# Performance work log

Hardware: AMD Instinct MI355X
Metric: run time of the kernel (lower is better)

The kernel has to match this reference:

```python
import jax, jax.numpy as jnp
import numpy as np

EPS_SHIFT = 1e-8   # additive epsilon used by the original code
EPS_NORM = 1e-12   # torch.nn.functional.normalize default eps


def setup_inputs() -> dict:
    key = jax.random.key(0)
    inputs = jax.random.normal(key, (1024, 2048, 3, 3), dtype=jnp.float32)
    return {"inputs": inputs}


def reference(inputs):
    # inputs: (B, num_res, 3, 3) -> flat atom chain (B, N, 3), N = 3*num_res
    B, R = inputs.shape[0], inputs.shape[1]
    x = inputs.reshape(B, R * 3, 3)

    # sliding 4-atom windows, vectorized over all N-3 dihedrals
    a = x[:, :-3, :]
    b = x[:, 1:-2, :]
    c = x[:, 2:-1, :]
    d = x[:, 3:, :]

    bc_raw = b - c + EPS_SHIFT
    bc = bc_raw / jnp.clip(
        jnp.linalg.norm(bc_raw, axis=-1, keepdims=True), EPS_NORM)

    n1 = jnp.cross(a - b, bc)          # (B, N-3, 3)
    n2 = jnp.cross(bc, c - d)          # (B, N-3, 3)
    xc = jnp.sum(n1 * n2, axis=-1)     # (B, N-3)
    yc = jnp.sum(jnp.cross(n1, bc) * n2, axis=-1)
    dih = jnp.arctan2(yc, xc + EPS_SHIFT)

    # original concatenates all sin values then all cos values along last dim
    angles = jnp.concatenate([jnp.sin(dih), jnp.cos(dih)], axis=-1)  # (B, 2*(N-3))
    first_three = x[:, :3, :]                                        # (B, 3, 3)
    return (angles, first_three)
```

## Files before the change

### kernel.cpp

```cpp
#include <hip/hip_runtime.h>

#define ROWS 1024
#define PTS 6144
#define NDIH (PTS - 3)
#define ROWF (PTS * 3)
#define CHUNK 256
#define NCHUNK ((NDIH + CHUNK - 1) / CHUNK)
#define ANG_PER_ROW (2 * NDIH)
#define EPS_SHIFT 1e-8f
#define EPS_NORM 1e-12f

__global__ __launch_bounds__(256) void dih_kernel(const float* __restrict__ in,
                                                  float* __restrict__ out) {
    __shared__ float s[(CHUNK + 3) * 3];
    const int b     = blockIdx.x / NCHUNK;
    const int chunk = blockIdx.x % NCHUNK;
    const int i0    = chunk * CHUNK;
    const int t     = threadIdx.x;

    const float* row = in + (size_t)b * ROWF;
    const int base = i0 * 3;
    const int cnt  = min((CHUNK + 3) * 3, ROWF - base);
    for (int k = t; k < cnt; k += CHUNK) s[k] = row[base + k];
    __syncthreads();

    if (chunk == 0 && t < 9) {
        out[(size_t)ROWS * ANG_PER_ROW + (size_t)b * 9 + t] = s[t];
    }

    const int i = i0 + t;
    if (i < NDIH) {
        const float* p = s + 3 * t;
        const float ax = p[0], ay = p[1],  az = p[2];
        const float bx = p[3], by = p[4],  bz = p[5];
        const float cx = p[6], cy = p[7],  cz = p[8];
        const float dx = p[9], dy = p[10], dz = p[11];

        const float brx = bx - cx + EPS_SHIFT;
        const float bry = by - cy + EPS_SHIFT;
        const float brz = bz - cz + EPS_SHIFT;
        const float nrm = sqrtf(brx*brx + bry*bry + brz*brz);
        const float inv = 1.0f / fmaxf(nrm, EPS_NORM);
        const float ux = brx * inv, uy = bry * inv, uz = brz * inv;

        const float abx = ax - bx, aby = ay - by, abz = az - bz;
        const float n1x = aby*uz - abz*uy;
        const float n1y = abz*ux - abx*uz;
        const float n1z = abx*uy - aby*ux;

        const float cdx = cx - dx, cdy = cy - dy, cdz = cz - dz;
        const float n2x = uy*cdz - uz*cdy;
        const float n2y = uz*cdx - ux*cdz;
        const float n2z = ux*cdy - uy*cdx;

        const float xc = n1x*n2x + n1y*n2y + n1z*n2z;

        const float mx = n1y*uz - n1z*uy;
        const float my = n1z*ux - n1x*uz;
        const float mz = n1x*uy - n1y*ux;
        const float yc = mx*n2x + my*n2y + mz*n2z;

        const float xz = xc + EPS_SHIFT;
        const float r2 = yc*yc + xz*xz;
        float s_, c_;
        if (r2 > 0.0f) {
            const float rinv = rsqrtf(r2);
            s_ = yc * rinv;
            c_ = xz * rinv;
        } else {
            s_ = 0.0f;
            c_ = 1.0f;
        }
        const size_t obase = (size_t)b * ANG_PER_ROW;
        out[obase + i]        = s_;
        out[obase + NDIH + i] = c_;
    }
}

extern "C" void kernel_launch(void* const* d_in, const int* in_sizes, int n_in,
                              void* d_out, int out_size, void* d_ws, size_t ws_size,
                              hipStream_t stream) {
    const float* in = (const float*)d_in[0];
    float* out = (float*)d_out;
    dih_kernel<<<dim3(ROWS * NCHUNK), dim3(CHUNK), 0, stream>>>(in, out);
}
```

Baseline: 139.5 us.

## Compute four dihedrals per thread with shared edge vectors and vectorized memory access

Each thread now computes four consecutive dihedrals from a 21-float register window. Bond differences are computed once and shared across adjacent dihedrals, and the chunk grows to 1024 dihedrals per 256-thread block. Global-to-shared staging and shared-to-register reads use float4, and sine outputs are written as float2 pairs. The aim is fewer instructions and memory transactions per dihedral, at the cost of higher register use per thread, fewer blocks, and a tail path for the last partial chunk.

```diff
diff --git a/kernel.cpp b/kernel.cpp
--- a/kernel.cpp
+++ b/kernel.cpp
@@ -4,15 +4,17 @@
 #define PTS 6144
 #define NDIH (PTS - 3)
 #define ROWF (PTS * 3)
-#define CHUNK 256
+#define CHUNK 1024
+#define DPT 4
+#define THREADS (CHUNK / DPT)
 #define NCHUNK ((NDIH + CHUNK - 1) / CHUNK)
 #define ANG_PER_ROW (2 * NDIH)
+#define SFLOATS ((CHUNK + 3) * 3 + 3)
 #define EPS_SHIFT 1e-8f
-#define EPS_NORM 1e-12f
 
 __global__ __launch_bounds__(256) void dih_kernel(const float* __restrict__ in,
                                                   float* __restrict__ out) {
-    __shared__ float s[(CHUNK + 3) * 3];
+    __shared__ float s[SFLOATS];
     const int b     = blockIdx.x / NCHUNK;
     const int chunk = blockIdx.x % NCHUNK;
     const int i0    = chunk * CHUNK;
@@ -20,41 +22,53 @@
 
     const float* row = in + (size_t)b * ROWF;
     const int base = i0 * 3;
-    const int cnt  = min((CHUNK + 3) * 3, ROWF - base);
-    for (int k = t; k < cnt; k += CHUNK) s[k] = row[base + k];
+    const int n4 = min(SFLOATS / 4, (ROWF - base) / 4);
+    const float4* g4 = (const float4*)(row + base);
+    float4* s4 = (float4*)s;
+    for (int k = t; k < n4; k += THREADS) s4[k] = g4[k];
     __syncthreads();
 
-    if (chunk == 0 && t < 9) {
+    if (chunk == 0 && t < 9)
         out[(size_t)ROWS * ANG_PER_ROW + (size_t)b * 9 + t] = s[t];
+
+    float w[21];
+    {
+        const float4* ls4 = (const float4*)(s + 12 * t);
+        float4 v0 = ls4[0], v1 = ls4[1], v2 = ls4[2], v3 = ls4[3], v4 = ls4[4];
+        w[0]=v0.x;  w[1]=v0.y;  w[2]=v0.z;  w[3]=v0.w;
+        w[4]=v1.x;  w[5]=v1.y;  w[6]=v1.z;  w[7]=v1.w;
+        w[8]=v2.x;  w[9]=v2.y;  w[10]=v2.z; w[11]=v2.w;
+        w[12]=v3.x; w[13]=v3.y; w[14]=v3.z; w[15]=v3.w;
+        w[16]=v4.x; w[17]=v4.y; w[18]=v4.z; w[19]=v4.w;
+        w[20]=s[12 * t + 20];
     }
 
-    const int i = i0 + t;
-    if (i < NDIH) {
-        const float* p = s + 3 * t;
-        const float ax = p[0], ay = p[1],  az = p[2];
-        const float bx = p[3], by = p[4],  bz = p[5];
-        const float cx = p[6], cy = p[7],  cz = p[8];
-        const float dx = p[9], dy = p[10], dz = p[11];
+    float ex[6], ey[6], ez[6];
+    #pragma unroll
+    for (int j = 0; j < 6; ++j) {
+        ex[j] = w[3*j + 0] - w[3*j + 3];
+        ey[j] = w[3*j + 1] - w[3*j + 4];
+        ez[j] = w[3*j + 2] - w[3*j + 5];
+    }
 
-        const float brx = bx - cx + EPS_SHIFT;
-        const float bry = by - cy + EPS_SHIFT;
-        const float brz = bz - cz + EPS_SHIFT;
-        const float nrm = sqrtf(brx*brx + bry*bry + brz*brz);
-        const float inv = 1.0f / fmaxf(nrm, EPS_NORM);
+    float sv[DPT], cv[DPT];
+    #pragma unroll
+    for (int k = 0; k < DPT; ++k) {
+        const float brx = ex[k+1] + EPS_SHIFT;
+        const float bry = ey[k+1] + EPS_SHIFT;
+        const float brz = ez[k+1] + EPS_SHIFT;
+        const float nrm2 = brx*brx + bry*bry + brz*brz;
+        const float inv = rsqrtf(fmaxf(nrm2, 1e-24f));
         const float ux = brx * inv, uy = bry * inv, uz = brz * inv;
 
-        const float abx = ax - bx, aby = ay - by, abz = az - bz;
-        const float n1x = aby*uz - abz*uy;
-        const float n1y = abz*ux - abx*uz;
-        const float n1z = abx*uy - aby*ux;
-
-        const float cdx = cx - dx, cdy = cy - dy, cdz = cz - dz;
-        const float n2x = uy*cdz - uz*cdy;
-        const float n2y = uz*cdx - ux*cdz;
-        const float n2z = ux*cdy - uy*cdx;
+        const float n1x = ey[k]*uz - ez[k]*uy;
+        const float n1y = ez[k]*ux - ex[k]*uz;
+        const float n1z = ex[k]*uy - ey[k]*ux;
+        const float n2x = uy*ez[k+2] - uz*ey[k+2];
+        const float n2y = uz*ex[k+2] - ux*ez[k+2];
+        const float n2z = ux*ey[k+2] - uy*ex[k+2];
 
         const float xc = n1x*n2x + n1y*n2y + n1z*n2z;
-
         const float mx = n1y*uz - n1z*uy;
         const float my = n1z*ux - n1x*uz;
         const float mz = n1x*uy - n1y*ux;
@@ -62,18 +76,27 @@
 
         const float xz = xc + EPS_SHIFT;
         const float r2 = yc*yc + xz*xz;
-        float s_, c_;
-        if (r2 > 0.0f) {
-            const float rinv = rsqrtf(r2);
-            s_ = yc * rinv;
-            c_ = xz * rinv;
-        } else {
-            s_ = 0.0f;
-            c_ = 1.0f;
+        const float rinv = rsqrtf(fmaxf(r2, 1e-30f));
+        sv[k] = (r2 > 0.0f) ? yc * rinv : 0.0f;
+        cv[k] = (r2 > 0.0f) ? xz * rinv : 1.0f;
+    }
+
+    const int i = i0 + DPT * t;
+    const size_t obase = (size_t)b * ANG_PER_ROW;
+    if (i + DPT - 1 < NDIH) {
+        float2* so = (float2*)(out + obase + i);
+        so[0] = make_float2(sv[0], sv[1]);
+        so[1] = make_float2(sv[2], sv[3]);
+        float* co = out + obase + NDIH + i;
+        co[0] = cv[0]; co[1] = cv[1]; co[2] = cv[2]; co[3] = cv[3];
+    } else {
+        #pragma unroll
+        for (int k = 0; k < DPT; ++k) {
+            if (i + k < NDIH) {
+                out[obase + i + k]        = sv[k];
+                out[obase + NDIH + i + k] = cv[k];
+            }
         }
-        const size_t obase = (size_t)b * ANG_PER_ROW;
-        out[obase + i]        = s_;
-        out[obase + NDIH + i] = c_;
     }
 }
 
@@ -82,5 +105,5 @@
                               hipStream_t stream) {
     const float* in = (const float*)d_in[0];
     float* out = (float*)d_out;
-    dih_kernel<<<dim3(ROWS * NCHUNK), dim3(CHUNK), 0, stream>>>(in, out);
+    dih_kernel<<<dim3(ROWS * NCHUNK), dim3(THREADS), 0, stream>>>(in, out);
 }
```

New measurement: 120.2 us. 13.8% less time.
